# Kernel tuning notes

Hardware: AMD Instinct MI355X
Metric: run time of the kernel (lower is better)

Reference implementation:

```python
import jax, jax.numpy as jnp
import numpy as np


def _gat(x, adj, W, a):
    # x: [N, J, Fin], W: [H, Fin, hs], a: [H, 2*hs]
    # e_ij = leakyrelu(a1.Wh_i + a2.Wh_j)  (decomposed form of the repeat/cat construction)
    hs = W.shape[-1]
    Wh = jnp.einsum('bjf,hfd->bhjd', x, W)
    s1 = jnp.einsum('bhjd,hd->bhj', Wh, a[:, :hs])
    s2 = jnp.einsum('bhjd,hd->bhj', Wh, a[:, hs:])
    e = jax.nn.leaky_relu(s1[..., :, None] + s2[..., None, :], 0.2)
    e = jnp.where(adj[None, None] > 0, e, jnp.float32(-9e15))
    att = jax.nn.softmax(e, axis=-1)
    h = jnp.einsum('bhij,bhjd->bhid', att, Wh)
    b, H, j, d = h.shape
    return jax.nn.elu(h.transpose(0, 2, 1, 3).reshape(b, j, H * d))


def _conv_bn_relu(x, w, bias, g, be, m, v):
    # x: [N, C, T], w: [O, I, 3], BN in inference mode
    y = jax.lax.conv_general_dilated(x, w, (1,), [(1, 1)], dimension_numbers=('NCH', 'OIH', 'NCH'))
    y = y + bias[None, :, None]
    y = (y - m[None, :, None]) / jnp.sqrt(v[None, :, None] + 1e-5) * g[None, :, None] + be[None, :, None]
    return jax.nn.relu(y)


def _mha(q, k, v, wq, bq, wk, bk, wv, bv, wo, bo):
    # torch nn.MultiheadAttention, 4 heads, eval mode (no dropout)
    n, L, D = q.shape
    H = 4
    hd = D // H
    def proj(x, w, b):
        return (x @ w.T + b).reshape(n, -1, H, hd)
    Q, K, V = proj(q, wq, bq), proj(k, wk, bk), proj(v, wv, bv)
    att = jax.nn.softmax(jnp.einsum('nqhd,nkhd->nhqk', Q, K) * jnp.float32(1.0 / np.sqrt(hd)), axis=-1)
    o = jnp.einsum('nhqk,nkhd->nqhd', att, V).reshape(n, L, D)
    return o @ wo.T + bo


def _lstm_dir(x, wih, whh, bih, bhh, rev):
    # x: [B, T, D]; torch gate order i, f, g, o
    b, t, _ = x.shape
    H = whh.shape[1]
    xw = jnp.transpose(x @ wih.T + (bih + bhh), (1, 0, 2))  # [T, B, 4H]
    def step(carry, xt):
        h, c = carry
        gates = xt + h @ whh.T
        i, f, g, o = jnp.split(gates, 4, axis=-1)
        c = jax.nn.sigmoid(f) * c + jax.nn.sigmoid(i) * jnp.tanh(g)
        h = jax.nn.sigmoid(o) * jnp.tanh(c)
        return (h, c), h
    init = (jnp.zeros((b, H), x.dtype), jnp.zeros((b, H), x.dtype))
    _, hs = jax.lax.scan(step, init, xw, reverse=rev)
    return jnp.transpose(hs, (1, 0, 2))


def _forward(lh, rh, adj, vis, g1W, g1a, g2W, g2a, c1w, c1b, b1g, b1b, b1m, b1v, c2w, c2b, b2g, b2b, b2m, b2v,
             wq, bq, wk, bk, wv, bv, wo, bo,
             l0fw, l0fu, l0fbi, l0fbh, l0bw, l0bu, l0bbi, l0bbh,
             l1fw, l1fu, l1fbi, l1fbh, l1bw, l1bu, l1bbi, l1bbh,
             o1w, o1b, o2w, o2b):
    B, T, J, F = lh.shape

    def single_hand(x):
        h = x.reshape(B * T, J, F)
        h = _gat(h, adj, g1W, g1a)
        h = _gat(h, adj, g2W, g2a)
        D = h.shape[-1]
        ht = h.reshape(B, T, J, D).transpose(0, 2, 3, 1).reshape(B * J, D, T)
        ht = _conv_bn_relu(ht, c1w, c1b, b1g, b1b, b1m, b1v)
        ht = _conv_bn_relu(ht, c2w, c2b, b2g, b2b, b2m, b2v)
        return ht.reshape(B, J, D, T).transpose(0, 3, 1, 2)  # [B, T, J, D]

    l = single_hand(lh)
    r = single_hand(rh)
    D = l.shape[-1]
    lf = l.reshape(B * T, J, D)
    rf = r.reshape(B * T, J, D)
    a_l2r = _mha(lf, rf, rf, wq, bq, wk, bk, wv, bv, wo, bo)
    a_r2l = _mha(rf, lf, lf, wq, bq, wk, bk, wv, bv, wo, bo)
    # repair of shape-inconsistent torch reshape: pool joints before the seq LSTM
    le = (lf + 0.5 * a_r2l).reshape(B, T, J, D).mean(axis=2)
    re = (rf + 0.5 * a_l2r).reshape(B, T, J, D).mean(axis=2)

    def bilstm(x):
        h1 = jnp.concatenate([_lstm_dir(x, l0fw, l0fu, l0fbi, l0fbh, False),
                              _lstm_dir(x, l0bw, l0bu, l0bbi, l0bbh, True)], -1)
        return jnp.concatenate([_lstm_dir(h1, l1fw, l1fu, l1fbi, l1fbh, False),
                                _lstm_dir(h1, l1bw, l1bu, l1bbi, l1bbh, True)], -1)

    def head(x):
        y = jax.nn.relu(x @ o1w.T + o1b) @ o2w.T + o2b  # [B, T, 3*J]
        return y.reshape(B, T, J, 3)

    lp = head(bilstm(le)) * vis[..., None]
    rp = head(bilstm(re)) * vis[..., None]
    return lp, rp


def setup_inputs() -> dict:
    key = jax.random.key(0)
    ks = jax.random.split(key, 60)
    it = iter(range(60))
    B, T, J, F, D = 8, 512, 21, 512, 256
    def nrm(shape, s=0.05):
        return jax.random.normal(ks[next(it)], shape, jnp.float32) * s
    inp = {}
    inp['left_hand_feats'] = nrm((B, T, J, F), 1.0)
    inp['right_hand_feats'] = nrm((B, T, J, F), 1.0)
    adj = (jax.random.uniform(ks[next(it)], (J, J)) < 0.3).astype(jnp.float32)
    inp['hand_adj_matrix'] = jnp.maximum(adj, jnp.eye(J, dtype=jnp.float32))
    inp['hand_visibility'] = jax.random.uniform(ks[next(it)], (B, T, J), jnp.float32)
    inp['gat1_W'] = nrm((4, F, 64)); inp['gat1_a'] = nrm((4, 128))
    inp['gat2_W'] = nrm((4, D, 64)); inp['gat2_a'] = nrm((4, 128))
    inp['conv1_w'] = nrm((D, D, 3)); inp['conv1_b'] = nrm((D,))
    inp['conv2_w'] = nrm((D, D, 3)); inp['conv2_b'] = nrm((D,))
    for p in ['bn1', 'bn2']:
        inp[p + '_g'] = jnp.ones((D,), jnp.float32)
        inp[p + '_b'] = jnp.zeros((D,), jnp.float32)
        inp[p + '_m'] = jnp.zeros((D,), jnp.float32)
        inp[p + '_v'] = jnp.ones((D,), jnp.float32)
    for p in ['attn_wq', 'attn_wk', 'attn_wv', 'attn_wo']:
        inp[p] = nrm((D, D))
    for p in ['attn_bq', 'attn_bk', 'attn_bv', 'attn_bo']:
        inp[p] = nrm((D,))
    H = D // 2
    for l in ['lstm0f', 'lstm0b', 'lstm1f', 'lstm1b']:
        inp[l + '_wih'] = nrm((4 * H, D))
        inp[l + '_whh'] = nrm((4 * H, H))
        inp[l + '_bih'] = nrm((4 * H,))
        inp[l + '_bhh'] = nrm((4 * H,))
    inp['out1_w'] = nrm((D, D)); inp['out1_b'] = nrm((D,))
    inp['out2_w'] = nrm((3 * J, D)); inp['out2_b'] = nrm((3 * J,))
    return inp


def reference(left_hand_feats, right_hand_feats, hand_adj_matrix, hand_visibility,
              gat1_W, gat1_a, gat2_W, gat2_a,
              conv1_w, conv1_b, bn1_g, bn1_b, bn1_m, bn1_v,
              conv2_w, conv2_b, bn2_g, bn2_b, bn2_m, bn2_v,
              attn_wq, attn_bq, attn_wk, attn_bk, attn_wv, attn_bv, attn_wo, attn_bo,
              lstm0f_wih, lstm0f_whh, lstm0f_bih, lstm0f_bhh,
              lstm0b_wih, lstm0b_whh, lstm0b_bih, lstm0b_bhh,
              lstm1f_wih, lstm1f_whh, lstm1f_bih, lstm1f_bhh,
              lstm1b_wih, lstm1b_whh, lstm1b_bih, lstm1b_bhh,
              out1_w, out1_b, out2_w, out2_b):
    return _forward(left_hand_feats, right_hand_feats, hand_adj_matrix, hand_visibility,
                    gat1_W, gat1_a, gat2_W, gat2_a,
                    conv1_w, conv1_b, bn1_g, bn1_b, bn1_m, bn1_v,
                    conv2_w, conv2_b, bn2_g, bn2_b, bn2_m, bn2_v,
                    attn_wq, attn_bq, attn_wk, attn_bk, attn_wv, attn_bv, attn_wo, attn_bo,
                    lstm0f_wih, lstm0f_whh, lstm0f_bih, lstm0f_bhh,
                    lstm0b_wih, lstm0b_whh, lstm0b_bih, lstm0b_bhh,
                    lstm1f_wih, lstm1f_whh, lstm1f_bih, lstm1f_bhh,
                    lstm1b_wih, lstm1b_whh, lstm1b_bih, lstm1b_bhh,
                    out1_w, out1_b, out2_w, out2_b)
```

## Files before the change

### kernel.cpp

```cpp
#include <hip/hip_runtime.h>

typedef __bf16 bf16;
typedef bf16 bf16x8 __attribute__((ext_vector_type(8)));
typedef bf16 bf16x4 __attribute__((ext_vector_type(4)));
typedef float f32x4 __attribute__((ext_vector_type(4)));
typedef _Float16 f16;
typedef f16 f16x8 __attribute__((ext_vector_type(8)));

#define NBT 4096
#define NJ 21
#define NLF 86016
#define DD 256
#define CONV_M 86352
#define SPAD 514
#define CROWS 86528

__device__ __forceinline__ void gload16(const bf16* g, bf16* l) {
  __builtin_amdgcn_global_load_lds(
      (const __attribute__((address_space(1))) unsigned int*)g,
      (__attribute__((address_space(3))) unsigned int*)l, 16, 0, 0);
}

__global__ __launch_bounds__(256, 2) void gemm_bf16(
    const void* __restrict__ Av, const bf16* __restrict__ Bt,
    float* __restrict__ C32, bf16* __restrict__ Cout,
    const float* __restrict__ bias, const float* __restrict__ sc,
    const float* __restrict__ sh, int M, int N, int K, int lda, int flags)
{
  __shared__ __align__(16) bf16 As[2][128][32];
  __shared__ __align__(16) bf16 Bs[2][128][32];
  const int tid = threadIdx.x;
  const long m0 = (long)blockIdx.y * 128;
  const int n0 = blockIdx.x * 128;
  const int wave = tid >> 6, lane = tid & 63;
  const int wm = (wave & 1) * 64, wn = (wave >> 1) * 64;
  const int frow = lane & 15, fkb = (lane >> 4) * 8;
  const int crow = lane >> 2, ccol = (lane & 3) * 8;
  const bf16* Ab = (const bf16*)Av;
  const int nk = K >> 5;
  const int ch0 = wave * 2, ch1 = ch0 + 1;
  const long arow0 = (m0 + ch0 * 16 + crow) * (long)lda + ccol;
  const long arow1 = (m0 + ch1 * 16 + crow) * (long)lda + ccol;
  const long brow0 = ((long)(n0 + ch0 * 16 + crow)) * K + ccol;
  const long brow1 = ((long)(n0 + ch1 * 16 + crow)) * K + ccol;

  f32x4 acc[4][4] = {};
  gload16(Ab + arow0, &As[0][ch0 * 16][0]);
  gload16(Ab + arow1, &As[0][ch1 * 16][0]);
  gload16(Bt + brow0, &Bs[0][ch0 * 16][0]);
  gload16(Bt + brow1, &Bs[0][ch1 * 16][0]);

  for (int kt = 0; kt < nk; kt++) {
    const int cur = kt & 1;
    if (kt + 1 < nk) {
      const int k0 = (kt + 1) << 5;
      gload16(Ab + arow0 + k0, &As[cur ^ 1][ch0 * 16][0]);
      gload16(Ab + arow1 + k0, &As[cur ^ 1][ch1 * 16][0]);
      gload16(Bt + brow0 + k0, &Bs[cur ^ 1][ch0 * 16][0]);
      gload16(Bt + brow1 + k0, &Bs[cur ^ 1][ch1 * 16][0]);
      asm volatile("s_waitcnt vmcnt(4) lgkmcnt(0)" ::: "memory");
    } else {
      asm volatile("s_waitcnt vmcnt(0) lgkmcnt(0)" ::: "memory");
    }
    __builtin_amdgcn_sched_barrier(0);
    __builtin_amdgcn_s_barrier();
    __builtin_amdgcn_sched_barrier(0);
    bf16x8 af[4], bg[4];
    #pragma unroll
    for (int i = 0; i < 4; i++) af[i] = *(const bf16x8*)(&As[cur][wm + i * 16 + frow][fkb]);
    #pragma unroll
    for (int j = 0; j < 4; j++) bg[j] = *(const bf16x8*)(&Bs[cur][wn + j * 16 + frow][fkb]);
    #pragma unroll
    for (int i = 0; i < 4; i++)
      #pragma unroll
      for (int j = 0; j < 4; j++)
        acc[i][j] = __builtin_amdgcn_mfma_f32_16x16x32_bf16(af[i], bg[j], acc[i][j], 0, 0, 0);
    asm volatile("s_waitcnt lgkmcnt(0)" ::: "memory");
    __builtin_amdgcn_sched_barrier(0);
    __builtin_amdgcn_s_barrier();
    __builtin_amdgcn_sched_barrier(0);
  }
  const int col = lane & 15, rbase = (lane >> 4) * 4;
  #pragma unroll
  for (int i = 0; i < 4; i++) {
    #pragma unroll
    for (int j = 0; j < 4; j++) {
      const int nn = n0 + wn + j * 16 + col;
      #pragma unroll
      for (int r = 0; r < 4; r++) {
        const long mm = m0 + wm + i * 16 + rbase + r;
        if (mm >= M) continue;
        float v = acc[i][j][r];
        if (flags & 2) { C32[mm * (long)N + nn] = v; continue; }
        if (flags & 8) v = v * sc[nn] + sh[nn];
        else if (bias) v += bias[nn];
        if (flags & 4) v = fmaxf(v, 0.f);
        if (flags & 16) {
          const int s = (int)(mm % SPAD);
          if (s == 0 || s == SPAD - 1) v = 0.f;
          Cout[mm * (long)N + nn] = (bf16)v;
        } else if (flags & 32) {
          const long hj = mm / SPAD; const int s = (int)(mm - hj * SPAD);
          if (s == 0 || s == SPAD - 1) continue;
          const long b = hj / NJ; const int j2 = (int)(hj - b * NJ);
          const long dst = (b * 512 + (s - 1)) * NJ + j2;
          Cout[dst * (long)N + nn] = (bf16)v;
        } else {
          Cout[mm * (long)N + nn] = (bf16)v;
        }
      }
    }
  }
}

__global__ void cvt_k(const float* __restrict__ s, bf16* __restrict__ d, long n) {
  long i = (long)blockIdx.x * 256 + threadIdx.x;
  if (i < n) d[i] = (bf16)s[i];
}
__global__ void cvt4_k(const float* __restrict__ s, bf16* __restrict__ d, long n4) {
  long i = (long)blockIdx.x * 256 + threadIdx.x;
  if (i >= n4) return;
  const f32x4 v = ((const f32x4*)s)[i];
  bf16x4 o; o[0] = (bf16)v[0]; o[1] = (bf16)v[1]; o[2] = (bf16)v[2]; o[3] = (bf16)v[3];
  ((bf16x4*)d)[i] = o;
}
__global__ void prep_gatW(const float* __restrict__ W, bf16* __restrict__ Wt, int F) {
  long idx = (long)blockIdx.x * 256 + threadIdx.x;
  if (idx >= 256L * F) return;
  int n = (int)(idx / F), f = (int)(idx % F);
  Wt[idx] = (bf16)W[((long)(n >> 6) * F + f) * 64 + (n & 63)];
}
__global__ void prep_convw(const float* __restrict__ w, bf16* __restrict__ wp) {
  int idx = blockIdx.x * 256 + threadIdx.x;
  int n = idx / 768, k = idx % 768, tap = k >> 8, i = k & 255;
  wp[idx] = (bf16)w[(n * 256 + i) * 3 + tap];
}
__global__ void prep_out2(const float* __restrict__ w, bf16* __restrict__ wp) {
  int idx = blockIdx.x * 256 + threadIdx.x;
  wp[idx] = (idx < 63 * 256) ? (bf16)w[idx] : (bf16)0.f;
}
__global__ void prep_scsh(const float* __restrict__ cb, const float* __restrict__ g,
                          const float* __restrict__ be, const float* __restrict__ m,
                          const float* __restrict__ v, float* __restrict__ sc,
                          float* __restrict__ sh) {
  int c = threadIdx.x;
  float rs = rsqrtf(v[c] + 1e-5f) * g[c];
  sc[c] = rs; sh[c] = (cb[c] - m[c]) * rs + be[c];
}
__global__ void prep_bkv(const float* __restrict__ bk, const float* __restrict__ bv,
                         float* __restrict__ o) {
  int i = blockIdx.x * 256 + threadIdx.x;
  if (i >= 512) return;
  o[i] = (i < 256) ? bk[i] : bv[i - 256];
}
__global__ void pad_zero(bf16* __restrict__ convIn) {
  int idx = blockIdx.x * 256 + threadIdx.x;
  int hj = idx >> 9, s = ((idx >> 8) & 1) ? (SPAD - 1) : 0, c = idx & 255;
  convIn[((long)hj * SPAD + s) * DD + c] = (bf16)0.f;
}
__global__ void zero_out(float* __restrict__ o, long n) {
  long i = (long)blockIdx.x * 256 + threadIdx.x;
  if (i < n) o[i] = 0.f;
}

__global__ __launch_bounds__(256) void gat_attn(
    const bf16* __restrict__ Wh, const float* __restrict__ a,
    const float* __restrict__ adj, bf16* __restrict__ out, int convMode)
{
  const int bt = blockIdx.x, tid = threadIdx.x;
  __shared__ float whs[NJ][DD];
  __shared__ float s1[4][NJ], s2[4][NJ];
  __shared__ float att[4][NJ][NJ];
  const long base = (long)bt * NJ * DD;
  for (int i = tid; i < NJ * DD; i += 256)
    whs[i >> 8][i & 255] = (float)Wh[base + i];
  __syncthreads();
  if (tid < 4 * NJ) {
    const int h = tid / NJ, i = tid % NJ;
    float x1 = 0.f, x2 = 0.f;
    for (int d = 0; d < 64; d++) {
      const float w = whs[i][h * 64 + d];
      x1 += w * a[h * 128 + d];
      x2 += w * a[h * 128 + 64 + d];
    }
    s1[h][i] = x1; s2[h][i] = x2;
  }
  __syncthreads();
  for (int idx = tid; idx < 4 * NJ * NJ; idx += 256) {
    const int h = idx / (NJ * NJ), r = idx % (NJ * NJ), i = r / NJ, j = r % NJ;
    float e = s1[h][i] + s2[h][j];
    e = e > 0.f ? e : 0.2f * e;
    att[h][i][j] = (adj[i * NJ + j] > 0.f) ? e : -9e15f;
  }
  __syncthreads();
  if (tid < 4 * NJ) {
    const int h = tid / NJ, i = tid % NJ;
    float mx = -3e38f;
    for (int j = 0; j < NJ; j++) mx = fmaxf(mx, att[h][i][j]);
    float sum = 0.f;
    for (int j = 0; j < NJ; j++) { const float ex = __expf(att[h][i][j] - mx); att[h][i][j] = ex; sum += ex; }
    const float inv = 1.f / sum;
    for (int j = 0; j < NJ; j++) att[h][i][j] *= inv;
  }
  __syncthreads();
  const int b = bt >> 9, t = bt & 511;
  for (int idx = tid; idx < NJ * DD; idx += 256) {
    const int i = idx >> 8, c = idx & 255, h = c >> 6;
    float s = 0.f;
    for (int j = 0; j < NJ; j++) s += att[h][i][j] * whs[j][c];
    s = s > 0.f ? s : (__expf(s) - 1.f);
    const long row = convMode ? (((long)(b * NJ + i)) * SPAD + (t + 1)) : ((long)bt * NJ + i);
    out[row * DD + c] = (bf16)s;
  }
}

__global__ __launch_bounds__(256) void mha_core2(
    const bf16* __restrict__ Q, const bf16* __restrict__ KV,
    bf16* __restrict__ O)
{
  const int bt = blockIdx.x, tid = threadIdx.x;
  __shared__ bf16 qs[NJ][DD], ks[NJ][DD], vs[NJ][DD];
  __shared__ float att[4][NJ][NJ];
  const long baseq = (long)bt * NJ * DD;
  const long basekv = (long)bt * NJ * 512;
  for (int i = tid; i < NJ * DD; i += 256) {
    const int r = i >> 8, c = i & 255;
    qs[r][c] = Q[baseq + i];
    ks[r][c] = KV[basekv + r * 512 + c];
    vs[r][c] = KV[basekv + r * 512 + 256 + c];
  }
  __syncthreads();
  for (int idx = tid; idx < 4 * NJ * NJ; idx += 256) {
    const int h = idx / (NJ * NJ), r = idx % (NJ * NJ), i = r / NJ, j = r % NJ;
    float s = 0.f;
    for (int d = 0; d < 64; d++) s += (float)qs[i][h * 64 + d] * (float)ks[j][h * 64 + d];
    att[h][i][j] = s * 0.125f;
  }
  __syncthreads();
  if (tid < 4 * NJ) {
    const int h = tid / NJ, i = tid % NJ;
    float mx = -3e38f;
    for (int j = 0; j < NJ; j++) mx = fmaxf(mx, att[h][i][j]);
    float sum = 0.f;
    for (int j = 0; j < NJ; j++) { const float ex = __expf(att[h][i][j] - mx); att[h][i][j] = ex; sum += ex; }
    const float inv = 1.f / sum;
    for (int j = 0; j < NJ; j++) att[h][i][j] *= inv;
  }
  __syncthreads();
  for (int idx = tid; idx < NJ * DD; idx += 256) {
    const int i = idx >> 8, c = idx & 255, h = c >> 6;
    float s = 0.f;
    for (int j = 0; j < NJ; j++) s += att[h][i][j] * (float)vs[j][c];
    O[baseq + i * DD + c] = (bf16)s;
  }
}

__global__ __launch_bounds__(256) void pool_kernel(
    const bf16* __restrict__ lf, const bf16* __restrict__ ao, bf16* __restrict__ o)
{
  const int bt = blockIdx.x, c = threadIdx.x;
  float s = 0.f;
  for (int j = 0; j < NJ; j++) {
    const long r = ((long)bt * NJ + j) * DD + c;
    s += (float)lf[r] + 0.5f * (float)ao[r];
  }
  o[(long)bt * DD + c] = (bf16)(s * (1.f / 21.f));
}

#define REP16(X) X(0) X(1) X(2) X(3) X(4) X(5) X(6) X(7) X(8) X(9) X(10) X(11) \
  X(12) X(13) X(14) X(15)

#define LDS_FENCE() do { \
  asm volatile("s_waitcnt lgkmcnt(0)" ::: "memory"); \
  __builtin_amdgcn_sched_barrier(0); \
  __builtin_amdgcn_s_barrier(); \
  __builtin_amdgcn_sched_barrier(0); \
} while (0)

__global__ __launch_bounds__(512, 1) void lstm_lds(
    const float* __restrict__ xw,
    const float* __restrict__ whhF, const float* __restrict__ whhB,
    const float* __restrict__ bihF, const float* __restrict__ bhhF,
    const float* __restrict__ bihB, const float* __restrict__ bhhB,
    bf16* __restrict__ outL, bf16* __restrict__ outR)
{
  const int wg = blockIdx.x;
  const int hand = wg >> 4, dir = (wg >> 3) & 1, b = wg & 7;
  const int tid = threadIdx.x;
  const float* whh = dir ? whhB : whhF;

  __shared__ f16 whhs[512][136];
  __shared__ f16 hbuf[136];
  __shared__ float gsb[512];

  for (int i = tid; i < 512 * 128; i += 512)
    whhs[i >> 7][i & 127] = (f16)whh[i];
  if (tid < 136) hbuf[tid] = (f16)0.f;
  const float bias = (dir ? bihB : bihF)[tid] + (dir ? bhhB : bhhF)[tid];
  float c = 0.f;
  const float* xp = xw + ((long)hand * NBT + (long)b * 512) * 1024 + dir * 512;
  bf16* outp = hand ? outR : outL;
  float xv = xp[(long)(dir ? 511 : 0) * 1024 + tid];
  __syncthreads();

  const f16* wrow = &whhs[tid][0];
#define WRD(i) f16x8 w##i = *(const f16x8*)(wrow + (i) * 8);
  REP16(WRD)
#undef WRD

  for (int s = 0; s < 512; s++) {
    const int t = dir ? (511 - s) : s;
    const int tn = dir ? (510 - s) : (s + 1);
    float xnext = 0.f;
    if (s < 511) xnext = xp[(long)tn * 1024 + tid];
    float a0 = xv + bias, a1 = 0.f, a2 = 0.f, a3 = 0.f;
#define WDOT(i) { \
    const f16x8 hv = *(const f16x8*)(&hbuf[(i) * 8]); \
    a0 = __builtin_amdgcn_fdot2(__builtin_shufflevector(w##i, w##i, 0, 1), \
                                __builtin_shufflevector(hv, hv, 0, 1), a0, false); \
    a1 = __builtin_amdgcn_fdot2(__builtin_shufflevector(w##i, w##i, 2, 3), \
                                __builtin_shufflevector(hv, hv, 2, 3), a1, false); \
    a2 = __builtin_amdgcn_fdot2(__builtin_shufflevector(w##i, w##i, 4, 5), \
                                __builtin_shufflevector(hv, hv, 4, 5), a2, false); \
    a3 = __builtin_amdgcn_fdot2(__builtin_shufflevector(w##i, w##i, 6, 7), \
                                __builtin_shufflevector(hv, hv, 6, 7), a3, false); }
    REP16(WDOT)
#undef WDOT
    gsb[tid] = (a0 + a1) + (a2 + a3);
    LDS_FENCE();
    if (tid < 128) {
      const float ig = gsb[tid], fg = gsb[tid + 128], gg = gsb[tid + 256], og = gsb[tid + 384];
      const float si = __builtin_amdgcn_rcpf(1.f + __expf(-ig));
      const float sf = __builtin_amdgcn_rcpf(1.f + __expf(-fg));
      const float so = __builtin_amdgcn_rcpf(1.f + __expf(-og));
      const float tg = 1.f - 2.f * __builtin_amdgcn_rcpf(1.f + __expf(2.f * gg));
      c = sf * c + si * tg;
      const float tc = 1.f - 2.f * __builtin_amdgcn_rcpf(1.f + __expf(2.f * c));
      const float h = so * tc;
      hbuf[tid] = (f16)h;
      outp[((long)b * 512 + t) * 256 + dir * 128 + tid] = (bf16)h;
    }
    LDS_FENCE();
    xv = xnext;
  }
}

__global__ __launch_bounds__(256) void finalize_k(
    const float* __restrict__ y, const float* __restrict__ b2,
    const float* __restrict__ vis, float* __restrict__ out)
{
  const int idx = blockIdx.x * 256 + threadIdx.x;
  if (idx >= 2 * NBT * 63) return;
  const int c = idx % 63; const int r = idx / 63; const int bt = r & (NBT - 1);
  out[idx] = (y[(long)r * 128 + c] + b2[c]) * vis[bt * 21 + (c / 3)];
}

extern "C" void kernel_launch(void* const* d_in, const int* in_sizes, int n_in,
                              void* d_out, int out_size, void* d_ws, size_t ws_size,
                              hipStream_t stream) {
  (void)in_sizes; (void)n_in;
  const float* feats[2] = { (const float*)d_in[0], (const float*)d_in[1] };
  const float* adj  = (const float*)d_in[2];
  const float* vis  = (const float*)d_in[3];
  const float* gW[2] = { (const float*)d_in[4], (const float*)d_in[6] };
  const float* ga[2] = { (const float*)d_in[5], (const float*)d_in[7] };
  const float* cw_[2] = { (const float*)d_in[8],  (const float*)d_in[10] };
  const float* cb_[2] = { (const float*)d_in[9],  (const float*)d_in[11] };
  const float* bng[2] = { (const float*)d_in[12], (const float*)d_in[16] };
  const float* bnb[2] = { (const float*)d_in[13], (const float*)d_in[17] };
  const float* bnm[2] = { (const float*)d_in[14], (const float*)d_in[18] };
  const float* bnv[2] = { (const float*)d_in[15], (const float*)d_in[19] };
  const float* wq = (const float*)d_in[20], *wk = (const float*)d_in[21];
  const float* wv = (const float*)d_in[22], *wo = (const float*)d_in[23];
  const float* bq = (const float*)d_in[24], *bk = (const float*)d_in[25];
  const float* bv = (const float*)d_in[26], *bo = (const float*)d_in[27];
  const float* Lwih[2][2] = { { (const float*)d_in[28], (const float*)d_in[32] },
                              { (const float*)d_in[36], (const float*)d_in[40] } };
  const float* Lwhh[2][2] = { { (const float*)d_in[29], (const float*)d_in[33] },
                              { (const float*)d_in[37], (const float*)d_in[41] } };
  const float* Lbih[2][2] = { { (const float*)d_in[30], (const float*)d_in[34] },
                              { (const float*)d_in[38], (const float*)d_in[42] } };
  const float* Lbhh[2][2] = { { (const float*)d_in[31], (const float*)d_in[35] },
                              { (const float*)d_in[39], (const float*)d_in[43] } };
  const float* o1w = (const float*)d_in[44], *o1b = (const float*)d_in[45];
  const float* o2w = (const float*)d_in[46], *o2b = (const float*)d_in[47];

  char* base = (char*)d_ws;
  size_t off = 0;
  auto alloc = [&](size_t b) { size_t r = off; off += (b + 1023) & ~(size_t)1023; return r; };
  const size_t SZ_LF  = (size_t)NLF * DD * 2;
  const size_t SZ_CNV = (size_t)CROWS * DD * 2;
  const size_t SZ_BT  = (size_t)NBT * DD * 2;
  const size_t o_w1t = alloc((size_t)256 * 512 * 2);
  const size_t o_w2t = alloc((size_t)256 * 256 * 2);
  const size_t o_cw1 = alloc((size_t)256 * 768 * 2);
  const size_t o_cw2 = alloc((size_t)256 * 768 * 2);
  const size_t o_wq  = alloc((size_t)256 * 256 * 2);
  const size_t o_wk  = alloc((size_t)256 * 256 * 2);
  const size_t o_wv  = alloc((size_t)256 * 256 * 2);
  const size_t o_wo  = alloc((size_t)256 * 256 * 2);
  const size_t o_o1w = alloc((size_t)256 * 256 * 2);
  const size_t o_o2p = alloc((size_t)128 * 256 * 2);
  const size_t o_lw0 = alloc((size_t)512 * 256 * 2);
  const size_t o_lw1 = alloc((size_t)512 * 256 * 2);
  const size_t o_lw2 = alloc((size_t)512 * 256 * 2);
  const size_t o_lw3 = alloc((size_t)512 * 256 * 2);
  const size_t o_ss  = alloc((size_t)4 * 256 * 4);
  const size_t o_bkv = alloc((size_t)512 * 4);
  const size_t o_B1  = alloc(SZ_LF);
  const size_t o_B23 = alloc(2 * SZ_CNV);
  const size_t o_lfL = alloc(SZ_LF);
  const size_t o_lfR = alloc(SZ_LF);
  const size_t o_le  = alloc(SZ_BT);
  const size_t o_re  = alloc(SZ_BT);
  const size_t o_h1L = alloc(SZ_BT);
  const size_t o_h1R = alloc(SZ_BT);
  const size_t o_hoL = alloc(SZ_BT);
  const size_t o_hoR = alloc(SZ_BT);
  const size_t NEED = off;
  if (ws_size < NEED) {
    zero_out<<<(out_size + 255) / 256, 256, 0, stream>>>((float*)d_out, out_size);
    return;
  }
  auto P = [&](size_t o_) { return (void*)(base + o_); };

  auto gemm = [&](const void* A, const void* Bt, void* c32, void* co,
                  const void* bias_, const void* sc_, const void* sh_,
                  long M, int N, int K, int lda, int flags) {
    dim3 g((unsigned)(N / 128), (unsigned)((M + 127) / 128));
    gemm_bf16<<<g, 256, 0, stream>>>(A, (const bf16*)Bt, (float*)c32, (bf16*)co,
                                     (const float*)bias_, (const float*)sc_,
                                     (const float*)sh_, (int)M, N, K, lda, flags);
  };
  auto cvt = [&](const float* s, void* d, long n) {
    cvt_k<<<(unsigned)((n + 255) / 256), 256, 0, stream>>>(s, (bf16*)d, n);
  };

  prep_gatW<<<512, 256, 0, stream>>>(gW[0], (bf16*)P(o_w1t), 512);
  prep_gatW<<<256, 256, 0, stream>>>(gW[1], (bf16*)P(o_w2t), 256);
  prep_convw<<<768, 256, 0, stream>>>(cw_[0], (bf16*)P(o_cw1));
  prep_convw<<<768, 256, 0, stream>>>(cw_[1], (bf16*)P(o_cw2));
  cvt(wq, P(o_wq), 65536); cvt(wk, P(o_wk), 65536);
  cvt(wv, P(o_wv), 65536); cvt(wo, P(o_wo), 65536);
  cvt(o1w, P(o_o1w), 65536);
  cvt(Lwih[0][0], P(o_lw0), 131072); cvt(Lwih[0][1], P(o_lw1), 131072);
  cvt(Lwih[1][0], P(o_lw2), 131072); cvt(Lwih[1][1], P(o_lw3), 131072);
  prep_out2<<<128, 256, 0, stream>>>(o2w, (bf16*)P(o_o2p));
  float* sc1 = (float*)P(o_ss); float* sh1 = sc1 + 256;
  float* sc2 = sh1 + 256;       float* sh2 = sc2 + 256;
  prep_scsh<<<1, 256, 0, stream>>>(cb_[0], bng[0], bnb[0], bnm[0], bnv[0], sc1, sh1);
  prep_scsh<<<1, 256, 0, stream>>>(cb_[1], bng[1], bnb[1], bnm[1], bnv[1], sc2, sh2);
  prep_bkv<<<2, 256, 0, stream>>>(bk, bv, (float*)P(o_bkv));

  bf16* B1 = (bf16*)P(o_B1);
  bf16* B2 = (bf16*)P(o_B23);
  bf16* B3 = B2 + (size_t)CROWS * DD;
  bf16* lfb[2] = { (bf16*)P(o_lfL), (bf16*)P(o_lfR) };

  for (int hd = 0; hd < 2; hd++) {
    bf16* featbf = B2;
    cvt4_k<<<(unsigned)(((long)NLF * 512 / 4 + 255) / 256), 256, 0, stream>>>(
        feats[hd], featbf, (long)NLF * 512 / 4);
    gemm(featbf, P(o_w1t), nullptr, B1, nullptr, nullptr, nullptr,
         NLF, 256, 512, 512, 0);
    gat_attn<<<NBT, 256, 0, stream>>>(B1, ga[0], adj, B1, 0);
    gemm(B1, P(o_w2t), nullptr, B2, nullptr, nullptr, nullptr,
         NLF, 256, 256, 256, 0);
    pad_zero<<<336, 256, 0, stream>>>(B3 + DD);
    gat_attn<<<NBT, 256, 0, stream>>>(B2, ga[1], adj, B3 + DD, 1);
    gemm(B3, P(o_cw1), nullptr, B2 + DD, nullptr, sc1, sh1,
         CONV_M, 256, 768, 256, 8 | 4 | 16);
    gemm(B2, P(o_cw2), nullptr, lfb[hd], nullptr, sc2, sh2,
         CONV_M, 256, 768, 256, 8 | 4 | 32);
  }

  bf16* KV = (bf16*)P(o_B23);
  for (int pass = 0; pass < 2; pass++) {
    const bf16* qsrc = lfb[pass];
    const bf16* kvsrc = lfb[1 - pass];
    gemm(kvsrc, P(o_wk), nullptr, KV, P(o_bkv), nullptr, nullptr,
         NLF, 512, 256, 256, 0);
    gemm(qsrc, P(o_wq), nullptr, B1, bq, nullptr, nullptr, NLF, 256, 256, 256, 0);
    mha_core2<<<NBT, 256, 0, stream>>>(B1, KV, B1);
    gemm(B1, P(o_wo), nullptr, B2, bo, nullptr, nullptr, NLF, 256, 256, 256, 0);
    pool_kernel<<<NBT, 256, 0, stream>>>(kvsrc, B2,
        (bf16*)P(pass == 0 ? o_re : o_le));
  }

  float* xw = (float*)P(o_B23);
  gemm(P(o_le), P(o_lw0), xw, nullptr, nullptr, nullptr, nullptr,
       2 * NBT, 1024, 256, 256, 2);
  lstm_lds<<<32, 512, 0, stream>>>(xw, Lwhh[0][0], Lwhh[0][1],
      Lbih[0][0], Lbhh[0][0], Lbih[0][1], Lbhh[0][1],
      (bf16*)P(o_h1L), (bf16*)P(o_h1R));
  gemm(P(o_h1L), P(o_lw2), xw, nullptr, nullptr, nullptr, nullptr,
       2 * NBT, 1024, 256, 256, 2);
  lstm_lds<<<32, 512, 0, stream>>>(xw, Lwhh[1][0], Lwhh[1][1],
      Lbih[1][0], Lbhh[1][0], Lbih[1][1], Lbhh[1][1],
      (bf16*)P(o_hoL), (bf16*)P(o_hoR));

  gemm(P(o_hoL), P(o_o1w), nullptr, B1, o1b, nullptr, nullptr,
       2 * NBT, 256, 256, 256, 4);
  float* y32 = (float*)P(o_B23);
  gemm(B1, P(o_o2p), y32, nullptr, nullptr, nullptr, nullptr,
       2 * NBT, 128, 256, 256, 2);
  finalize_k<<<(2 * NBT * 63 + 255) / 256, 256, 0, stream>>>(
      y32, o2b, vis, (float*)d_out);
}
```

Before: 2.229 ms.

## Batch both hands through GAT/conv pipeline and fuse fp32-to-bf16 input conversion into GEMM

Removes the separate fp32-to-bf16 conversion pass over the input features. The first GEMM now reads fp32 A directly and converts while staging into LDS. The left and right hand pipelines (GAT attention, second GAT GEMM, both conv GEMMs) are merged into single launches over doubled row counts, with index math updated for the hand offset. This cuts launch count and improves GPU fill, at the cost of larger workspace buffers and a synchronous per-thread fp32 A load path that no longer uses async global-to-LDS loads.

After: 2.129 ms. 4.5% less time.

```diff
diff --git a/kernel.cpp b/kernel.cpp
--- a/kernel.cpp
+++ b/kernel.cpp
@@ -2,7 +2,6 @@
 
 typedef __bf16 bf16;
 typedef bf16 bf16x8 __attribute__((ext_vector_type(8)));
-typedef bf16 bf16x4 __attribute__((ext_vector_type(4)));
 typedef float f32x4 __attribute__((ext_vector_type(4)));
 typedef _Float16 f16;
 typedef f16 f16x8 __attribute__((ext_vector_type(8)));
@@ -11,9 +10,10 @@
 #define NJ 21
 #define NLF 86016
 #define DD 256
-#define CONV_M 86352
+#define CONVM1 86352
+#define CONVM2 172704
 #define SPAD 514
-#define CROWS 86528
+#define CROWS_ALL 173056
 
 __device__ __forceinline__ void gload16(const bf16* g, bf16* l) {
   __builtin_amdgcn_global_load_lds(
@@ -37,16 +37,30 @@
   const int frow = lane & 15, fkb = (lane >> 4) * 8;
   const int crow = lane >> 2, ccol = (lane & 3) * 8;
   const bf16* Ab = (const bf16*)Av;
+  const float* Af = (const float*)Av;
   const int nk = K >> 5;
   const int ch0 = wave * 2, ch1 = ch0 + 1;
   const long arow0 = (m0 + ch0 * 16 + crow) * (long)lda + ccol;
   const long arow1 = (m0 + ch1 * 16 + crow) * (long)lda + ccol;
   const long brow0 = ((long)(n0 + ch0 * 16 + crow)) * K + ccol;
   const long brow1 = ((long)(n0 + ch1 * 16 + crow)) * K + ccol;
+  const int lr = tid >> 1, lc = (tid & 1) * 16;
+
+  auto stageA_f32 = [&](int buf, int k0) {
+    const float* ap = Af + (m0 + lr) * (long)lda + (k0 + lc);
+    bf16x8 t0, t1;
+    #pragma unroll
+    for (int u = 0; u < 8; u++) { t0[u] = (bf16)ap[u]; t1[u] = (bf16)ap[8 + u]; }
+    *(bf16x8*)(&As[buf][lr][lc])     = t0;
+    *(bf16x8*)(&As[buf][lr][lc + 8]) = t1;
+  };
 
   f32x4 acc[4][4] = {};
-  gload16(Ab + arow0, &As[0][ch0 * 16][0]);
-  gload16(Ab + arow1, &As[0][ch1 * 16][0]);
+  if (flags & 1) stageA_f32(0, 0);
+  else {
+    gload16(Ab + arow0, &As[0][ch0 * 16][0]);
+    gload16(Ab + arow1, &As[0][ch1 * 16][0]);
+  }
   gload16(Bt + brow0, &Bs[0][ch0 * 16][0]);
   gload16(Bt + brow1, &Bs[0][ch1 * 16][0]);
 
@@ -54,11 +68,18 @@
     const int cur = kt & 1;
     if (kt + 1 < nk) {
       const int k0 = (kt + 1) << 5;
-      gload16(Ab + arow0 + k0, &As[cur ^ 1][ch0 * 16][0]);
-      gload16(Ab + arow1 + k0, &As[cur ^ 1][ch1 * 16][0]);
-      gload16(Bt + brow0 + k0, &Bs[cur ^ 1][ch0 * 16][0]);
-      gload16(Bt + brow1 + k0, &Bs[cur ^ 1][ch1 * 16][0]);
-      asm volatile("s_waitcnt vmcnt(4) lgkmcnt(0)" ::: "memory");
+      if (flags & 1) {
+        stageA_f32(cur ^ 1, k0);
+        gload16(Bt + brow0 + k0, &Bs[cur ^ 1][ch0 * 16][0]);
+        gload16(Bt + brow1 + k0, &Bs[cur ^ 1][ch1 * 16][0]);
+        asm volatile("s_waitcnt vmcnt(2) lgkmcnt(0)" ::: "memory");
+      } else {
+        gload16(Ab + arow0 + k0, &As[cur ^ 1][ch0 * 16][0]);
+        gload16(Ab + arow1 + k0, &As[cur ^ 1][ch1 * 16][0]);
+        gload16(Bt + brow0 + k0, &Bs[cur ^ 1][ch0 * 16][0]);
+        gload16(Bt + brow1 + k0, &Bs[cur ^ 1][ch1 * 16][0]);
+        asm volatile("s_waitcnt vmcnt(4) lgkmcnt(0)" ::: "memory");
+      }
     } else {
       asm volatile("s_waitcnt vmcnt(0) lgkmcnt(0)" ::: "memory");
     }
@@ -102,8 +123,9 @@
         } else if (flags & 32) {
           const long hj = mm / SPAD; const int s = (int)(mm - hj * SPAD);
           if (s == 0 || s == SPAD - 1) continue;
-          const long b = hj / NJ; const int j2 = (int)(hj - b * NJ);
-          const long dst = (b * 512 + (s - 1)) * NJ + j2;
+          const int hand = (int)(hj / 168); const int lhj = (int)(hj - hand * 168);
+          const int b = lhj / NJ; const int j2 = lhj - b * NJ;
+          const long dst = (long)hand * NLF + ((long)b * 512 + (s - 1)) * NJ + j2;
           Cout[dst * (long)N + nn] = (bf16)v;
         } else {
           Cout[mm * (long)N + nn] = (bf16)v;
@@ -116,13 +138,6 @@
 __global__ void cvt_k(const float* __restrict__ s, bf16* __restrict__ d, long n) {
   long i = (long)blockIdx.x * 256 + threadIdx.x;
   if (i < n) d[i] = (bf16)s[i];
-}
-__global__ void cvt4_k(const float* __restrict__ s, bf16* __restrict__ d, long n4) {
-  long i = (long)blockIdx.x * 256 + threadIdx.x;
-  if (i >= n4) return;
-  const f32x4 v = ((const f32x4*)s)[i];
-  bf16x4 o; o[0] = (bf16)v[0]; o[1] = (bf16)v[1]; o[2] = (bf16)v[2]; o[3] = (bf16)v[3];
-  ((bf16x4*)d)[i] = o;
 }
 __global__ void prep_gatW(const float* __restrict__ W, bf16* __restrict__ Wt, int F) {
   long idx = (long)blockIdx.x * 256 + threadIdx.x;
@@ -203,13 +218,15 @@
     for (int j = 0; j < NJ; j++) att[h][i][j] *= inv;
   }
   __syncthreads();
-  const int b = bt >> 9, t = bt & 511;
+  const int hand = bt >> 12, b = (bt >> 9) & 7, t = bt & 511;
   for (int idx = tid; idx < NJ * DD; idx += 256) {
     const int i = idx >> 8, c = idx & 255, h = c >> 6;
     float s = 0.f;
     for (int j = 0; j < NJ; j++) s += att[h][i][j] * whs[j][c];
     s = s > 0.f ? s : (__expf(s) - 1.f);
-    const long row = convMode ? (((long)(b * NJ + i)) * SPAD + (t + 1)) : ((long)bt * NJ + i);
+    const long row = convMode
+        ? ((long)hand * CONVM1 + ((long)(b * NJ + i)) * SPAD + (t + 1))
+        : ((long)bt * NJ + i);
     out[row * DD + c] = (bf16)s;
   }
 }
@@ -388,8 +405,7 @@
   char* base = (char*)d_ws;
   size_t off = 0;
   auto alloc = [&](size_t b) { size_t r = off; off += (b + 1023) & ~(size_t)1023; return r; };
-  const size_t SZ_LF  = (size_t)NLF * DD * 2;
-  const size_t SZ_CNV = (size_t)CROWS * DD * 2;
+  const size_t SZ_BIG = (size_t)CROWS_ALL * DD * 2;
   const size_t SZ_BT  = (size_t)NBT * DD * 2;
   const size_t o_w1t = alloc((size_t)256 * 512 * 2);
   const size_t o_w2t = alloc((size_t)256 * 256 * 2);
@@ -407,10 +423,10 @@
   const size_t o_lw3 = alloc((size_t)512 * 256 * 2);
   const size_t o_ss  = alloc((size_t)4 * 256 * 4);
   const size_t o_bkv = alloc((size_t)512 * 4);
-  const size_t o_B1  = alloc(SZ_LF);
-  const size_t o_B23 = alloc(2 * SZ_CNV);
-  const size_t o_lfL = alloc(SZ_LF);
-  const size_t o_lfR = alloc(SZ_LF);
+  const size_t o_BA  = alloc(SZ_BIG);
+  const size_t o_BH  = alloc(SZ_BIG);
+  const size_t o_lfL = alloc((size_t)NLF * DD * 2);
+  const size_t o_lfR = alloc((size_t)NLF * DD * 2);
   const size_t o_le  = alloc(SZ_BT);
   const size_t o_re  = alloc(SZ_BT);
   const size_t o_h1L = alloc(SZ_BT);
@@ -452,42 +468,37 @@
   prep_scsh<<<1, 256, 0, stream>>>(cb_[1], bng[1], bnb[1], bnm[1], bnv[1], sc2, sh2);
   prep_bkv<<<2, 256, 0, stream>>>(bk, bv, (float*)P(o_bkv));
 
-  bf16* B1 = (bf16*)P(o_B1);
-  bf16* B2 = (bf16*)P(o_B23);
-  bf16* B3 = B2 + (size_t)CROWS * DD;
+  bf16* BA = (bf16*)P(o_BA);
+  bf16* BH = (bf16*)P(o_BH);
   bf16* lfb[2] = { (bf16*)P(o_lfL), (bf16*)P(o_lfR) };
 
-  for (int hd = 0; hd < 2; hd++) {
-    bf16* featbf = B2;
-    cvt4_k<<<(unsigned)(((long)NLF * 512 / 4 + 255) / 256), 256, 0, stream>>>(
-        feats[hd], featbf, (long)NLF * 512 / 4);
-    gemm(featbf, P(o_w1t), nullptr, B1, nullptr, nullptr, nullptr,
-         NLF, 256, 512, 512, 0);
-    gat_attn<<<NBT, 256, 0, stream>>>(B1, ga[0], adj, B1, 0);
-    gemm(B1, P(o_w2t), nullptr, B2, nullptr, nullptr, nullptr,
-         NLF, 256, 256, 256, 0);
-    pad_zero<<<336, 256, 0, stream>>>(B3 + DD);
-    gat_attn<<<NBT, 256, 0, stream>>>(B2, ga[1], adj, B3 + DD, 1);
-    gemm(B3, P(o_cw1), nullptr, B2 + DD, nullptr, sc1, sh1,
-         CONV_M, 256, 768, 256, 8 | 4 | 16);
-    gemm(B2, P(o_cw2), nullptr, lfb[hd], nullptr, sc2, sh2,
-         CONV_M, 256, 768, 256, 8 | 4 | 32);
-  }
-
-  bf16* KV = (bf16*)P(o_B23);
+  for (int hd = 0; hd < 2; hd++)
+    gemm(feats[hd], P(o_w1t), nullptr, BA + (size_t)hd * NLF * DD,
+         nullptr, nullptr, nullptr, NLF, 256, 512, 512, 1);
+  gat_attn<<<2 * NBT, 256, 0, stream>>>(BA, ga[0], adj, BA, 0);
+  gemm(BA, P(o_w2t), nullptr, BH, nullptr, nullptr, nullptr,
+       2 * NLF, 256, 256, 256, 0);
+  pad_zero<<<672, 256, 0, stream>>>(BA + DD);
+  gat_attn<<<2 * NBT, 256, 0, stream>>>(BH, ga[1], adj, BA + DD, 1);
+  gemm(BA, P(o_cw1), nullptr, BH + DD, nullptr, sc1, sh1,
+       CONVM2, 256, 768, 256, 8 | 4 | 16);
+  gemm(BH, P(o_cw2), nullptr, lfb[0], nullptr, sc2, sh2,
+       CONVM2, 256, 768, 256, 8 | 4 | 32);
+
+  bf16* Bwo = BA + (size_t)NLF * DD;
   for (int pass = 0; pass < 2; pass++) {
     const bf16* qsrc = lfb[pass];
     const bf16* kvsrc = lfb[1 - pass];
-    gemm(kvsrc, P(o_wk), nullptr, KV, P(o_bkv), nullptr, nullptr,
+    gemm(kvsrc, P(o_wk), nullptr, BH, P(o_bkv), nullptr, nullptr,
          NLF, 512, 256, 256, 0);
-    gemm(qsrc, P(o_wq), nullptr, B1, bq, nullptr, nullptr, NLF, 256, 256, 256, 0);
-    mha_core2<<<NBT, 256, 0, stream>>>(B1, KV, B1);
-    gemm(B1, P(o_wo), nullptr, B2, bo, nullptr, nullptr, NLF, 256, 256, 256, 0);
-    pool_kernel<<<NBT, 256, 0, stream>>>(kvsrc, B2,
+    gemm(qsrc, P(o_wq), nullptr, BA, bq, nullptr, nullptr, NLF, 256, 256, 256, 0);
+    mha_core2<<<NBT, 256, 0, stream>>>(BA, BH, BA);
+    gemm(BA, P(o_wo), nullptr, Bwo, bo, nullptr, nullptr, NLF, 256, 256, 256, 0);
+    pool_kernel<<<NBT, 256, 0, stream>>>(kvsrc, Bwo,
         (bf16*)P(pass == 0 ? o_re : o_le));
   }
 
-  float* xw = (float*)P(o_B23);
+  float* xw = (float*)P(o_BH);
   gemm(P(o_le), P(o_lw0), xw, nullptr, nullptr, nullptr, nullptr,
        2 * NBT, 1024, 256, 256, 2);
   lstm_lds<<<32, 512, 0, stream>>>(xw, Lwhh[0][0], Lwhh[0][1],
@@ -499,10 +510,10 @@
       Lbih[1][0], Lbhh[1][0], Lbih[1][1], Lbhh[1][1],
       (bf16*)P(o_hoL), (bf16*)P(o_hoR));
 
-  gemm(P(o_hoL), P(o_o1w), nullptr, B1, o1b, nullptr, nullptr,
+  gemm(P(o_hoL), P(o_o1w), nullptr, BA, o1b, nullptr, nullptr,
        2 * NBT, 256, 256, 256, 4);
-  float* y32 = (float*)P(o_B23);
-  gemm(B1, P(o_o2p), y32, nullptr, nullptr, nullptr, nullptr,
+  float* y32 = (float*)P(o_BH);
+  gemm(BA, P(o_o2p), y32, nullptr, nullptr, nullptr, nullptr,
        2 * NBT, 128, 256, 256, 2);
   finalize_k<<<(2 * NBT * 63 + 255) / 256, 256, 0, stream>>>(
       y32, o2b, vis, (float*)d_out);
```
